# Optimization experiments

Hardware: AMD Instinct MI355X
Metric: run time of the kernel (lower is better)

Reference implementation:

```python
import jax, jax.numpy as jnp
import numpy as np

M, N, F = 512, 128, 512  # molecules, atoms per molecule, feature dim
HID, OUT = F // 4, 1


def setup_inputs() -> dict:
    key = jax.random.key(0)
    k1, k2, k3 = jax.random.split(key, 3)
    h = jax.random.normal(k1, (M, N, F), dtype=jnp.float32)
    W1 = jax.random.normal(k2, (F, HID), dtype=jnp.float32) * (1.0 / np.sqrt(F))
    b1 = jnp.zeros((HID,), dtype=jnp.float32)
    W2 = jax.random.normal(k3, (HID, OUT), dtype=jnp.float32) * (1.0 / np.sqrt(HID))
    b2 = jnp.zeros((OUT,), dtype=jnp.float32)
    return {"h": h, "W1": W1, "b1": b1, "W2": W2, "b2": b2}


def reference(h, W1, b1, W2, b2):
    # method == 'weighted_summation'
    # gate MLP: Linear -> ReLU -> Linear -> Sigmoid, per atom
    w = jax.nn.sigmoid(jax.nn.relu(h @ W1 + b1) @ W2 + b2)  # [M, N, OUT]
    # per-molecule weighted sum over atoms: mm(w_h.T, h) for each molecule,
    # concatenated along dim 0 -> [M*OUT, F] (OUT=1 -> [M, F])
    out = jnp.einsum('mno,mnf->mof', w, h)  # [M, OUT, F]
    return out.reshape(M * OUT, F)
```

## Files before the change

### kernel.cpp

```cpp
#include <hip/hip_runtime.h>
#include <hip/hip_bf16.h>


typedef unsigned short u16;
typedef unsigned int u32;
typedef __bf16 bf16x8 __attribute__((ext_vector_type(8)));
typedef float f32x4 __attribute__((ext_vector_type(4)));
typedef float f32x2 __attribute__((ext_vector_type(2)));
typedef u32 u32x4 __attribute__((ext_vector_type(4)));

#define M_MOL 512
#define N_ATOM 128
#define F_DIM 512
#define HID_DIM 128
#define ABLK 64
#define NBLK (M_MOL * 2)

static __device__ __forceinline__ u16 f2bf(float x) {
  u32 u = __float_as_uint(x);
  u32 r = (u + 0x7fffu + ((u >> 16) & 1u)) >> 16;
  return (u16)r;
}
static __device__ __forceinline__ bf16x8 pack8(u32x4 a, u32x4 b) {
  u32x4 r;
  r[0] = (a[0] >> 16) | (a[1] & 0xffff0000u);
  r[1] = (a[2] >> 16) | (a[3] & 0xffff0000u);
  r[2] = (b[0] >> 16) | (b[1] & 0xffff0000u);
  r[3] = (b[2] >> 16) | (b[3] & 0xffff0000u);
  return __builtin_bit_cast(bf16x8, r);
}

__global__ __launch_bounds__(256) void transpose_w1(const float* __restrict__ W1,
                                                    u16* __restrict__ W1Tt) {
  __shared__ float tile[64][65];
  const int k0 = blockIdx.x * 64;
  const int n0 = blockIdx.y * 64;
  const int t = threadIdx.x;
  #pragma unroll
  for (int i = 0; i < 16; ++i) {
    const int lin = i * 256 + t;
    const int lr = lin >> 6, lc = lin & 63;
    tile[lc][lr] = W1[(size_t)(k0 + lr) * HID_DIM + (n0 + lc)];
  }
  __syncthreads();
  #pragma unroll
  for (int i = 0; i < 16; ++i) {
    const int lin = i * 256 + t;
    const int wr = lin >> 6, wc = lin & 63;
    const int k = k0 + wc;
    W1Tt[(size_t)(k >> 5) * (HID_DIM * 32) + (size_t)(n0 + wr) * 32 + (k & 31)] =
        f2bf(tile[wr][wc]);
  }
}

__global__ __launch_bounds__(256, 2) void pool_partial(
    const float* __restrict__ h, const u16* __restrict__ W1Tt,
    const float* __restrict__ b1, const float* __restrict__ W2,
    const float* __restrict__ b2, float* __restrict__ part) {
  __shared__ u16 As[ABLK * F_DIM];
  __shared__ float w_s[ABLK];
  __shared__ float red[4][F_DIM];

  const int blk = blockIdx.x;
  const int tid = threadIdx.x;
  const int wv = tid >> 6;
  const int lane = tid & 63;
  const int quad = lane >> 4;
  const int cl = lane & 15;

  u16* AsW = As + wv * (16 * F_DIM);

  {
    const float* hw = h + (size_t)blk * (ABLK * F_DIM) + (size_t)(wv * 16) * F_DIM;
    #pragma unroll
    for (int g = 0; g < 4; ++g) {
      u32x4 lo[4], hi[4];
      #pragma unroll
      for (int i2 = 0; i2 < 4; ++i2) {
        const int i = g * 4 + i2;
        const u32x4* src = (const u32x4*)(hw + (size_t)i * F_DIM) + 2 * lane;
        lo[i2] = src[0];
        hi[i2] = src[1];
      }
      #pragma unroll
      for (int i2 = 0; i2 < 4; ++i2) {
        const int i = g * 4 + i2;
        const int phys = (lane & ~7) | ((lane ^ i) & 7);
        *(bf16x8*)(AsW + i * F_DIM + phys * 8) = pack8(lo[i2], hi[i2]);
      }
    }
  }

  const u16* bg = W1Tt + cl * 32 + quad * 8;
  u32x4 bA[8], bB[8];
  #pragma unroll
  for (int t = 0; t < 8; ++t) bA[t] = *(const u32x4*)(bg + t * 512);

  asm volatile("s_waitcnt lgkmcnt(0)" ::: "memory");
  __builtin_amdgcn_sched_barrier(0);

  f32x4 acc[8];
  #pragma unroll
  for (int t = 0; t < 8; ++t) acc[t] = (f32x4){0.f, 0.f, 0.f, 0.f};

  const u16* aBase = AsW + cl * F_DIM;

  #pragma unroll
  for (int ks = 0; ks < 16; ++ks) {
    const int c = ks * 4 + quad;
    const int aphys = (c & ~7) | ((c ^ cl) & 7);
    bf16x8 afr = *(const bf16x8*)(aBase + aphys * 8);
    if (ks < 15) {
      const u16* nb = bg + (size_t)(ks + 1) * (HID_DIM * 32);
      #pragma unroll
      for (int t = 0; t < 8; ++t) {
        u32x4 v = *(const u32x4*)(nb + t * 512);
        if (ks & 1) bA[t] = v; else bB[t] = v;
      }
    }
    #pragma unroll
    for (int t = 0; t < 8; ++t) {
      u32x4 bv = (ks & 1) ? bB[t] : bA[t];
      acc[t] = __builtin_amdgcn_mfma_f32_16x16x32_bf16(
          afr, __builtin_bit_cast(bf16x8, bv), acc[t], 0, 0, 0);
    }
  }

  float psum[4] = {0.f, 0.f, 0.f, 0.f};
  #pragma unroll
  for (int t = 0; t < 8; ++t) {
    const int hid = t * 16 + cl;
    const float b1v = b1[hid];
    const float w2v = W2[hid];
    #pragma unroll
    for (int r = 0; r < 4; ++r) {
      float tv = fmaxf(acc[t][r] + b1v, 0.f);
      psum[r] = fmaf(tv, w2v, psum[r]);
    }
  }
  #pragma unroll
  for (int off = 1; off < 16; off <<= 1)
    #pragma unroll
    for (int r = 0; r < 4; ++r)
      psum[r] += __shfl_xor(psum[r], off, 64);
  if (cl == 0) {
    const float b2v = b2[0];
    #pragma unroll
    for (int r = 0; r < 4; ++r)
      w_s[wv * 16 + quad * 4 + r] = 1.f / (1.f + __expf(-(psum[r] + b2v)));
  }
  asm volatile("s_waitcnt lgkmcnt(0)" ::: "memory");
  __builtin_amdgcn_sched_barrier(0);

  float facc[8] = {0.f, 0.f, 0.f, 0.f, 0.f, 0.f, 0.f, 0.f};
  #pragma unroll 4
  for (int i = 0; i < 16; ++i) {
    const float wn = w_s[wv * 16 + i];
    const int phys = (lane & ~7) | ((lane ^ i) & 7);
    bf16x8 hv = *(const bf16x8*)(AsW + i * F_DIM + phys * 8);
    u32x4 uv = __builtin_bit_cast(u32x4, hv);
    #pragma unroll
    for (int j = 0; j < 4; ++j) {
      facc[2 * j]     = fmaf(wn, __uint_as_float(uv[j] << 16), facc[2 * j]);
      facc[2 * j + 1] = fmaf(wn, __uint_as_float(uv[j] & 0xffff0000u), facc[2 * j + 1]);
    }
  }
  #pragma unroll
  for (int j = 0; j < 8; ++j) red[wv][lane * 8 + j] = facc[j];
  __syncthreads();

  {
    const int f = tid * 2;
    f32x2 o;
    o[0] = red[0][f] + red[1][f] + red[2][f] + red[3][f];
    o[1] = red[0][f + 1] + red[1][f + 1] + red[2][f + 1] + red[3][f + 1];
    *(f32x2*)(part + (size_t)blk * F_DIM + f) = o;
  }
}

__global__ __launch_bounds__(256) void reduce_out(const float* __restrict__ part,
                                                  float* __restrict__ out) {
  const int m = blockIdx.x;
  const int f = threadIdx.x * 2;
  f32x2 a = *(const f32x2*)(part + (size_t)(2 * m) * F_DIM + f);
  f32x2 b = *(const f32x2*)(part + (size_t)(2 * m + 1) * F_DIM + f);
  f32x2 o;
  o[0] = a[0] + b[0];
  o[1] = a[1] + b[1];
  *(f32x2*)(out + (size_t)m * F_DIM + f) = o;
}

extern "C" void kernel_launch(void* const* d_in, const int* in_sizes, int n_in,
                              void* d_out, int out_size, void* d_ws, size_t ws_size,
                              hipStream_t stream) {
  const float* h  = (const float*)d_in[0];
  const float* W1 = (const float*)d_in[1];
  const float* b1 = (const float*)d_in[2];
  const float* W2 = (const float*)d_in[3];
  const float* b2 = (const float*)d_in[4];
  float* out = (float*)d_out;

  u16* W1Tt = (u16*)d_ws;
  float* part = (float*)((char*)d_ws + (size_t)HID_DIM * F_DIM * sizeof(u16));

  transpose_w1<<<dim3(8, 2), 256, 0, stream>>>(W1, W1Tt);
  pool_partial<<<NBLK, 256, 0, stream>>>(h, W1Tt, b1, W2, b2, part);
  reduce_out<<<M_MOL, 256, 0, stream>>>(part, out);
}
```

Measured before the change: 215.9 us.

## Split each block's atoms across 8 waves and drop B-fragment double buffering

```diff
diff --git a/kernel.cpp b/kernel.cpp
--- a/kernel.cpp
+++ b/kernel.cpp
@@ -53,13 +53,12 @@
   }
 }
 
-__global__ __launch_bounds__(256, 2) void pool_partial(
+__global__ __launch_bounds__(512, 4) void pool_partial(
     const float* __restrict__ h, const u16* __restrict__ W1Tt,
     const float* __restrict__ b1, const float* __restrict__ W2,
     const float* __restrict__ b2, float* __restrict__ part) {
-  __shared__ u16 As[ABLK * F_DIM];
+  __shared__ __align__(16) u16 As[ABLK * F_DIM];
   __shared__ float w_s[ABLK];
-  __shared__ float red[4][F_DIM];
 
   const int blk = blockIdx.x;
   const int tid = threadIdx.x;
@@ -68,12 +67,12 @@
   const int quad = lane >> 4;
   const int cl = lane & 15;
 
-  u16* AsW = As + wv * (16 * F_DIM);
+  u16* AsW = As + wv * (8 * F_DIM);
 
   {
-    const float* hw = h + (size_t)blk * (ABLK * F_DIM) + (size_t)(wv * 16) * F_DIM;
-    #pragma unroll
-    for (int g = 0; g < 4; ++g) {
+    const float* hw = h + (size_t)blk * (ABLK * F_DIM) + (size_t)(wv * 8) * F_DIM;
+    #pragma unroll
+    for (int g = 0; g < 2; ++g) {
       u32x4 lo[4], hi[4];
       #pragma unroll
       for (int i2 = 0; i2 < 4; ++i2) {
@@ -92,9 +91,6 @@
   }
 
   const u16* bg = W1Tt + cl * 32 + quad * 8;
-  u32x4 bA[8], bB[8];
-  #pragma unroll
-  for (int t = 0; t < 8; ++t) bA[t] = *(const u32x4*)(bg + t * 512);
 
   asm volatile("s_waitcnt lgkmcnt(0)" ::: "memory");
   __builtin_amdgcn_sched_barrier(0);
@@ -103,27 +99,21 @@
   #pragma unroll
   for (int t = 0; t < 8; ++t) acc[t] = (f32x4){0.f, 0.f, 0.f, 0.f};
 
-  const u16* aBase = AsW + cl * F_DIM;
+  const u16* aBase = AsW + (cl & 7) * F_DIM;
 
   #pragma unroll
   for (int ks = 0; ks < 16; ++ks) {
+    u32x4 bfr[8];
+    #pragma unroll
+    for (int t = 0; t < 8; ++t)
+      bfr[t] = *(const u32x4*)(bg + (size_t)ks * (HID_DIM * 32) + t * 512);
     const int c = ks * 4 + quad;
     const int aphys = (c & ~7) | ((c ^ cl) & 7);
     bf16x8 afr = *(const bf16x8*)(aBase + aphys * 8);
-    if (ks < 15) {
-      const u16* nb = bg + (size_t)(ks + 1) * (HID_DIM * 32);
-      #pragma unroll
-      for (int t = 0; t < 8; ++t) {
-        u32x4 v = *(const u32x4*)(nb + t * 512);
-        if (ks & 1) bA[t] = v; else bB[t] = v;
-      }
-    }
-    #pragma unroll
-    for (int t = 0; t < 8; ++t) {
-      u32x4 bv = (ks & 1) ? bB[t] : bA[t];
+    #pragma unroll
+    for (int t = 0; t < 8; ++t)
       acc[t] = __builtin_amdgcn_mfma_f32_16x16x32_bf16(
-          afr, __builtin_bit_cast(bf16x8, bv), acc[t], 0, 0, 0);
-    }
+          afr, __builtin_bit_cast(bf16x8, bfr[t]), acc[t], 0, 0, 0);
   }
 
   float psum[4] = {0.f, 0.f, 0.f, 0.f};
@@ -143,19 +133,19 @@
     #pragma unroll
     for (int r = 0; r < 4; ++r)
       psum[r] += __shfl_xor(psum[r], off, 64);
-  if (cl == 0) {
+  if (cl == 0 && quad < 2) {
     const float b2v = b2[0];
     #pragma unroll
     for (int r = 0; r < 4; ++r)
-      w_s[wv * 16 + quad * 4 + r] = 1.f / (1.f + __expf(-(psum[r] + b2v)));
+      w_s[wv * 8 + quad * 4 + r] = 1.f / (1.f + __expf(-(psum[r] + b2v)));
   }
   asm volatile("s_waitcnt lgkmcnt(0)" ::: "memory");
   __builtin_amdgcn_sched_barrier(0);
 
   float facc[8] = {0.f, 0.f, 0.f, 0.f, 0.f, 0.f, 0.f, 0.f};
-  #pragma unroll 4
-  for (int i = 0; i < 16; ++i) {
-    const float wn = w_s[wv * 16 + i];
+  #pragma unroll
+  for (int i = 0; i < 8; ++i) {
+    const float wn = w_s[wv * 8 + i];
     const int phys = (lane & ~7) | ((lane ^ i) & 7);
     bf16x8 hv = *(const bf16x8*)(AsW + i * F_DIM + phys * 8);
     u32x4 uv = __builtin_bit_cast(u32x4, hv);
@@ -165,16 +155,19 @@
       facc[2 * j + 1] = fmaf(wn, __uint_as_float(uv[j] & 0xffff0000u), facc[2 * j + 1]);
     }
   }
-  #pragma unroll
-  for (int j = 0; j < 8; ++j) red[wv][lane * 8 + j] = facc[j];
+
+  float* red = (float*)As;
   __syncthreads();
+  #pragma unroll
+  for (int j = 0; j < 8; ++j) red[wv * F_DIM + lane * 8 + j] = facc[j];
+  __syncthreads();
 
   {
-    const int f = tid * 2;
-    f32x2 o;
-    o[0] = red[0][f] + red[1][f] + red[2][f] + red[3][f];
-    o[1] = red[0][f + 1] + red[1][f + 1] + red[2][f + 1] + red[3][f + 1];
-    *(f32x2*)(part + (size_t)blk * F_DIM + f) = o;
+    const int f = tid;
+    float o = 0.f;
+    #pragma unroll
+    for (int w = 0; w < 8; ++w) o += red[w * F_DIM + f];
+    part[(size_t)blk * F_DIM + f] = o;
   }
 }
 
@@ -204,6 +197,6 @@
   float* part = (float*)((char*)d_ws + (size_t)HID_DIM * F_DIM * sizeof(u16));
 
   transpose_w1<<<dim3(8, 2), 256, 0, stream>>>(W1, W1Tt);
-  pool_partial<<<NBLK, 256, 0, stream>>>(h, W1Tt, b1, W2, b2, part);
+  pool_partial<<<NBLK, 512, 0, stream>>>(h, W1Tt, b1, W2, b2, part);
   reduce_out<<<M_MOL, 256, 0, stream>>>(part, out);
 }
```

Result: slower. 241.8 us (+12.0%).
